# Kernel optimization log

Measured on AMD Instinct MI355X. Metric: run time of the kernel, lower is better.

Reference implementation:

```python
import jax, jax.numpy as jnp
import numpy as np
import math

N_HEADS = 16
D_EMBED = 1024
D_CROSS = 768
FF_DIM = 4096
D_HEAD = D_EMBED // N_HEADS
LN_EPS = 1e-5


def layer_norm(h, g, b):
    mu = jnp.mean(h, axis=-1, keepdims=True)
    var = jnp.var(h, axis=-1, keepdims=True)
    return (h - mu) * jax.lax.rsqrt(var + LN_EPS) * g + b


def mha(q, k, v):
    # q: [B,Sq,D], k/v: [B,Skv,D] -> split heads, attend, merge
    B, Sq, _ = q.shape
    Skv = k.shape[1]
    qh = q.reshape(B, Sq, N_HEADS, D_HEAD).transpose(0, 2, 1, 3)
    kh = k.reshape(B, Skv, N_HEADS, D_HEAD).transpose(0, 2, 1, 3)
    vh = v.reshape(B, Skv, N_HEADS, D_HEAD).transpose(0, 2, 1, 3)
    scores = jnp.einsum('bhqd,bhkd->bhqk', qh, kh) / math.sqrt(D_HEAD)
    attn = jax.nn.softmax(scores, axis=-1)
    out = jnp.einsum('bhqk,bhkd->bhqd', attn, vh)
    return out.transpose(0, 2, 1, 3).reshape(B, Sq, D_EMBED)


def setup_inputs() -> dict:
    key = jax.random.key(0)
    ks = jax.random.split(key, 24)
    s = 0.02
    inp = {
        'x': jax.random.normal(ks[0], (4, 1024, D_EMBED), jnp.float32),
        'y': jax.random.normal(ks[1], (4, 77, D_CROSS), jnp.float32),
        # self-attention in_proj (d_embed -> 3*d_embed) and out_proj
        'w_qkv': jax.random.normal(ks[2], (D_EMBED, 3 * D_EMBED), jnp.float32) * s,
        'b_qkv': jnp.zeros((3 * D_EMBED,), jnp.float32),
        'w_so': jax.random.normal(ks[3], (D_EMBED, D_EMBED), jnp.float32) * s,
        'b_so': jnp.zeros((D_EMBED,), jnp.float32),
        # cross-attention projections
        'w_q': jax.random.normal(ks[4], (D_EMBED, D_EMBED), jnp.float32) * s,
        'b_q': jnp.zeros((D_EMBED,), jnp.float32),
        'w_k': jax.random.normal(ks[5], (D_CROSS, D_EMBED), jnp.float32) * s,
        'b_k': jnp.zeros((D_EMBED,), jnp.float32),
        'w_v': jax.random.normal(ks[6], (D_CROSS, D_EMBED), jnp.float32) * s,
        'b_v': jnp.zeros((D_EMBED,), jnp.float32),
        'w_co': jax.random.normal(ks[7], (D_EMBED, D_EMBED), jnp.float32) * s,
        'b_co': jnp.zeros((D_EMBED,), jnp.float32),
        # 3-layer FFN
        'w1': jax.random.normal(ks[8], (D_EMBED, FF_DIM), jnp.float32) * s,
        'b1': jnp.zeros((FF_DIM,), jnp.float32),
        'w2': jax.random.normal(ks[9], (FF_DIM, FF_DIM), jnp.float32) * s,
        'b2': jnp.zeros((FF_DIM,), jnp.float32),
        'w3': jax.random.normal(ks[10], (FF_DIM, D_EMBED), jnp.float32) * s,
        'b3': jnp.zeros((D_EMBED,), jnp.float32),
        # single shared LayerNorm (used 3 times, as in the torch module)
        'ln_g': jnp.ones((D_EMBED,), jnp.float32),
        'ln_b': jnp.zeros((D_EMBED,), jnp.float32),
    }
    return inp


def reference(x, y, w_qkv, b_qkv, w_so, b_so, w_q, b_q, w_k, b_k, w_v, b_v,
              w_co, b_co, w1, b1, w2, b2, w3, b3, ln_g, ln_b):
    # --- self attention (no causal mask) ---
    qkv = x @ w_qkv + b_qkv
    q, k, v = jnp.split(qkv, 3, axis=-1)
    sa = mha(q, k, v) @ w_so + b_so
    x = layer_norm(x + sa, ln_g, ln_b)
    # --- cross attention ---
    qc = x @ w_q + b_q
    kc = y @ w_k + b_k
    vc = y @ w_v + b_v
    ca = mha(qc, kc, vc) @ w_co + b_co
    x = layer_norm(x + ca, ln_g, ln_b)
    # --- 3-layer FFN with ReLU ---
    h = jax.nn.relu(x @ w1 + b1)
    h = jax.nn.relu(h @ w2 + b2)
    ff = h @ w3 + b3
    x = layer_norm(x + ff, ln_g, ln_b)
    return x
```

## Files before the change

kernel.cpp:

```cpp
#include <hip/hip_runtime.h>
#include <hip/hip_bf16.h>
#include <math.h>

typedef short v8s __attribute__((ext_vector_type(8)));
typedef short v4s __attribute__((ext_vector_type(4)));
typedef float v4f __attribute__((ext_vector_type(4)));

__device__ __forceinline__ unsigned short f2bf(float f) {
  union { float f; unsigned u; } a; a.f = f;
  unsigned u = a.u + 0x7fffu + ((a.u >> 16) & 1u);
  return (unsigned short)(u >> 16);
}

__device__ __forceinline__ void gld_lds16(const unsigned short* g, unsigned short* l) {
  __builtin_amdgcn_global_load_lds(
      (const __attribute__((address_space(1))) void*)g,
      (__attribute__((address_space(3))) void*)l,
      16, 0, 0);
}

__global__ void cvt_f32_bf16(const float* __restrict__ in,
                             unsigned short* __restrict__ out, int n4) {
  int i = blockIdx.x * blockDim.x + threadIdx.x;
  if (i >= n4) return;
  float4 v = reinterpret_cast<const float4*>(in)[i];
  ushort4 o;
  o.x = f2bf(v.x); o.y = f2bf(v.y); o.z = f2bf(v.z); o.w = f2bf(v.w);
  reinterpret_cast<ushort4*>(out)[i] = o;
}

__global__ void cvt_transpose(const float* __restrict__ in,
                              unsigned short* __restrict__ out, int K, int N) {
  __shared__ float t[32][33];
  int bx = blockIdx.x, by = blockIdx.y;
  int tx = threadIdx.x, ty = threadIdx.y;
#pragma unroll
  for (int i = 0; i < 4; i++) {
    int k = by * 32 + ty + i * 8;
    t[ty + i * 8][tx] = in[(size_t)k * N + bx * 32 + tx];
  }
  __syncthreads();
#pragma unroll
  for (int i = 0; i < 4; i++) {
    int n = bx * 32 + ty + i * 8;
    out[(size_t)n * K + by * 32 + tx] = f2bf(t[tx][ty + i * 8]);
  }
}

__global__ __launch_bounds__(256)
void transpose_v(const unsigned short* __restrict__ V,
                 unsigned short* __restrict__ Vt,
                 int rowstride, int batch_rows, int Skv, int kvpad) {
  __shared__ __align__(16) unsigned short t[64][80];
  int ch = blockIdx.x, h = blockIdx.y, b = blockIdx.z;
  int tid = threadIdx.x;
  int sr = tid >> 2, sc = (tid & 3) * 16;
  int gr = ch * 64 + sr;
  v8s v0 = {}, v1 = {};
  if (gr < Skv) {
    const unsigned short* p = V + (size_t)(b * batch_rows + gr) * rowstride + h * 64 + sc;
    v0 = *(const v8s*)p; v1 = *(const v8s*)(p + 8);
  }
  *(v8s*)&t[sr][sc]     = v0;
  *(v8s*)&t[sr][sc + 8] = v1;
  __syncthreads();
  int d  = tid >> 2;
  int k0 = (tid & 3) * 16;
  unsigned short* o = Vt + ((size_t)(b * 16 + h) * 64 + d) * kvpad + ch * 64 + k0;
  v8s o0, o1;
#pragma unroll
  for (int e = 0; e < 8; e++) { o0[e] = t[k0 + e][d]; o1[e] = t[k0 + 8 + e][d]; }
  *(v8s*)o       = o0;
  *(v8s*)(o + 8) = o1;
}

template<bool RELU, bool OUTF, bool OUTB>
__global__ __launch_bounds__(256)
void gemm_bf16(const unsigned short* __restrict__ A,
               const unsigned short* __restrict__ BT,
               const float* __restrict__ bias,
               float* __restrict__ Cf, float* __restrict__ Cf2,
               unsigned short* __restrict__ Cb,
               int M, int N, int Kred, int ld) {
  __shared__ __align__(16) unsigned short lA[128 * 64];
  __shared__ __align__(16) unsigned short lB[128 * 64];
  int tid  = threadIdx.x;
  int lane = tid & 63;
  int wave = tid >> 6;
  int wr = (wave >> 1) * 64;
  int wc = (wave & 1) * 64;
  int quad = lane >> 4;
  int l15  = lane & 15;
  int m0 = blockIdx.y * 128;
  int n0 = blockIdx.x * 128;
  int z  = blockIdx.z;

  const unsigned short* Az = A  + (size_t)z * Kred;
  const unsigned short* Bz = BT + (size_t)z * Kred;
  float* Cfo = z ? Cf2 : Cf;
  const float* biasz = z ? nullptr : bias;

  int srow   = tid >> 3;
  int schunk = (tid & 7) ^ (srow & 7);
  const unsigned short* gA = Az + (size_t)(m0 + srow) * ld + schunk * 8;
  const unsigned short* gB = Bz + (size_t)(n0 + srow) * ld + schunk * 8;
  unsigned short* ldsA = lA + wave * 512;
  unsigned short* ldsB = lB + wave * 512;
  const size_t rowblk = (size_t)32 * ld;

  const v4f vzero = {0.f, 0.f, 0.f, 0.f};
  v4f acc[4][4];
#pragma unroll
  for (int i = 0; i < 4; i++)
#pragma unroll
    for (int j = 0; j < 4; j++) acc[i][j] = vzero;

  for (int k0 = 0; k0 < Kred; k0 += 64) {
#pragma unroll
    for (int i = 0; i < 4; i++) {
      gld_lds16(gA + k0 + i * rowblk, ldsA + i * 2048);
      gld_lds16(gB + k0 + i * rowblk, ldsB + i * 2048);
    }
    __syncthreads();
#pragma unroll
    for (int s = 0; s < 2; s++) {
      v8s aF[4], bF[4];
#pragma unroll
      for (int i = 0; i < 4; i++)
        aF[i] = *(const v8s*)&lA[(wr + i * 16 + l15) * 64 + (((s * 4 + quad) ^ (l15 & 7)) * 8)];
#pragma unroll
      for (int j = 0; j < 4; j++)
        bF[j] = *(const v8s*)&lB[(wc + j * 16 + l15) * 64 + (((s * 4 + quad) ^ (l15 & 7)) * 8)];
#pragma unroll
      for (int i = 0; i < 4; i++)
#pragma unroll
        for (int j = 0; j < 4; j++)
          acc[i][j] = __builtin_amdgcn_mfma_f32_16x16x32_bf16(aF[i], bF[j], acc[i][j], 0, 0, 0);
    }
    __syncthreads();
  }

#pragma unroll
  for (int j = 0; j < 4; j++) {
    int col = n0 + wc + j * 16 + l15;
    float bv = biasz ? biasz[col] : 0.f;
#pragma unroll
    for (int i = 0; i < 4; i++) {
#pragma unroll
      for (int r = 0; r < 4; r++) {
        int row = m0 + wr + i * 16 + quad * 4 + r;
        if (row < M) {
          float v = acc[i][j][r] + bv;
          if (RELU) v = fmaxf(v, 0.f);
          if (OUTF) Cfo[(size_t)row * N + col] = v;
          if (OUTB && !z) Cb[(size_t)row * N + col] = f2bf(v);
        }
      }
    }
  }
}

__global__ __launch_bounds__(256)
void attn_kernel(const unsigned short* __restrict__ Q,
                 const unsigned short* __restrict__ K,
                 const unsigned short* __restrict__ Vt,
                 unsigned short* __restrict__ O,
                 int q_rowstride, int kv_rowstride, int o_rowstride,
                 int q_batch_rows, int kv_batch_rows, int Skv, int kvpad,
                 float scale) {
  __shared__ __align__(16) unsigned short lK[64][72];
  __shared__ __align__(16) unsigned short lV[64][72];
  __shared__ __align__(16) unsigned short lP[4][16][72];
  int tid  = threadIdx.x;
  int lane = tid & 63;
  int wave = tid >> 6;
  int quad = lane >> 4;
  int l15  = lane & 15;
  int qt = blockIdx.x, h = blockIdx.y, b = blockIdx.z;

  const unsigned short* Qb  = Q  + (size_t)b * q_batch_rows * q_rowstride + h * 64;
  const unsigned short* Kb  = K  + (size_t)b * kv_batch_rows * kv_rowstride + h * 64;
  const unsigned short* Vtb = Vt + ((size_t)(b * 16 + h) * 64) * kvpad;

  v8s qf0, qf1;
  {
    const unsigned short* qr = Qb + (size_t)(qt * 64 + wave * 16 + l15) * q_rowstride + quad * 8;
    qf0 = *(const v8s*)(qr);
    qf1 = *(const v8s*)(qr + 32);
  }

  const v4f vzero = {0.f, 0.f, 0.f, 0.f};
  v4f o_acc[4];
#pragma unroll
  for (int t = 0; t < 4; t++) o_acc[t] = vzero;
  float m_r[4], l_r[4];
#pragma unroll
  for (int r = 0; r < 4; r++) { m_r[r] = -1e30f; l_r[r] = 0.f; }

  int sr = tid >> 2;
  int sc = (tid & 3) * 16;

  int nch = (Skv + 63) >> 6;
  for (int ch = 0; ch < nch; ch++) {
    int base = ch * 64;
    int gr = base + sr;
    v8s k0v = {}, k1v = {};
    if (gr < Skv) {
      const unsigned short* kp = Kb + (size_t)gr * kv_rowstride + sc;
      k0v = *(const v8s*)kp;  k1v = *(const v8s*)(kp + 8);
    }
    const unsigned short* vp = Vtb + (size_t)sr * kvpad + base + sc;
    v8s w0 = *(const v8s*)vp;
    v8s w1 = *(const v8s*)(vp + 8);
    __syncthreads();
    *(v8s*)&lK[sr][sc]     = k0v;
    *(v8s*)&lK[sr][sc + 8] = k1v;
    {
      v4s a0 = {w0[0], w0[1], w0[2], w0[3]};
      v4s a1 = {w0[4], w0[5], w0[6], w0[7]};
      v4s a2 = {w1[0], w1[1], w1[2], w1[3]};
      v4s a3 = {w1[4], w1[5], w1[6], w1[7]};
      *(v4s*)&lV[sr][sc]      = a0;
      *(v4s*)&lV[sr][sc + 4]  = a1;
      *(v4s*)&lV[sr][sc + 8]  = a2;
      *(v4s*)&lV[sr][sc + 12] = a3;
    }
    __syncthreads();

    float s[4][4];
#pragma unroll
    for (int t = 0; t < 4; t++) {
      v8s kf0 = *(const v8s*)&lK[t * 16 + l15][quad * 8];
      v8s kf1 = *(const v8s*)&lK[t * 16 + l15][32 + quad * 8];
      v4f sacc = vzero;
      sacc = __builtin_amdgcn_mfma_f32_16x16x32_bf16(qf0, kf0, sacc, 0, 0, 0);
      sacc = __builtin_amdgcn_mfma_f32_16x16x32_bf16(qf1, kf1, sacc, 0, 0, 0);
      int kvpos = base + t * 16 + l15;
      bool ok = kvpos < Skv;
#pragma unroll
      for (int r = 0; r < 4; r++) s[t][r] = ok ? sacc[r] * scale : -1e30f;
    }

#pragma unroll
    for (int r = 0; r < 4; r++) {
      float mx = fmaxf(fmaxf(s[0][r], s[1][r]), fmaxf(s[2][r], s[3][r]));
#pragma unroll
      for (int d = 1; d < 16; d <<= 1) mx = fmaxf(mx, __shfl_xor(mx, d));
      float mnew = fmaxf(m_r[r], mx);
      float alpha = __expf(m_r[r] - mnew);
      float sm = 0.f;
#pragma unroll
      for (int t = 0; t < 4; t++) { s[t][r] = __expf(s[t][r] - mnew); sm += s[t][r]; }
#pragma unroll
      for (int d = 1; d < 16; d <<= 1) sm += __shfl_xor(sm, d);
      l_r[r] = l_r[r] * alpha + sm;
      m_r[r] = mnew;
#pragma unroll
      for (int t = 0; t < 4; t++) o_acc[t][r] *= alpha;
    }

#pragma unroll
    for (int t = 0; t < 4; t++)
#pragma unroll
      for (int r = 0; r < 4; r++)
        lP[wave][quad * 4 + r][t * 16 + l15] = f2bf(s[t][r]);
    v8s pf0 = *(const v8s*)&lP[wave][l15][quad * 8];
    v8s pf1 = *(const v8s*)&lP[wave][l15][32 + quad * 8];
#pragma unroll
    for (int t = 0; t < 4; t++) {
      v8s vf0 = *(const v8s*)&lV[t * 16 + l15][quad * 8];
      v8s vf1 = *(const v8s*)&lV[t * 16 + l15][32 + quad * 8];
      o_acc[t] = __builtin_amdgcn_mfma_f32_16x16x32_bf16(pf0, vf0, o_acc[t], 0, 0, 0);
      o_acc[t] = __builtin_amdgcn_mfma_f32_16x16x32_bf16(pf1, vf1, o_acc[t], 0, 0, 0);
    }
  }

  int orow0 = b * q_batch_rows + qt * 64 + wave * 16;
#pragma unroll
  for (int t = 0; t < 4; t++) {
#pragma unroll
    for (int r = 0; r < 4; r++) {
      float v = o_acc[t][r] / l_r[r];
      O[(size_t)(orow0 + quad * 4 + r) * o_rowstride + h * 64 + t * 16 + l15] = f2bf(v);
    }
  }
}

__global__ __launch_bounds__(256)
void ln_kernel(const float* base, const float* __restrict__ delta,
               const float* __restrict__ delta2,
               const float* __restrict__ g, const float* __restrict__ bb,
               float* outf, unsigned short* __restrict__ outb) {
  __shared__ float red[8];
  int row = blockIdx.x;
  int tid = threadIdx.x;
  float4 vb = ((const float4*)(base  + (size_t)row * 1024))[tid];
  float4 vd = ((const float4*)(delta + (size_t)row * 1024))[tid];
  float v0 = vb.x + vd.x, v1 = vb.y + vd.y, v2 = vb.z + vd.z, v3 = vb.w + vd.w;
  if (delta2) {
    float4 v2d = ((const float4*)(delta2 + (size_t)row * 1024))[tid];
    v0 += v2d.x; v1 += v2d.y; v2 += v2d.z; v3 += v2d.w;
  }
  float s = v0 + v1 + v2 + v3;
  float q = v0 * v0 + v1 * v1 + v2 * v2 + v3 * v3;
#pragma unroll
  for (int d = 1; d < 64; d <<= 1) { s += __shfl_xor(s, d); q += __shfl_xor(q, d); }
  int wave = tid >> 6, lane = tid & 63;
  if (lane == 0) { red[wave] = s; red[4 + wave] = q; }
  __syncthreads();
  s = red[0] + red[1] + red[2] + red[3];
  q = red[4] + red[5] + red[6] + red[7];
  float mean = s * (1.f / 1024.f);
  float var  = q * (1.f / 1024.f) - mean * mean;
  float rstd = rsqrtf(var + 1e-5f);
  float4 gg  = ((const float4*)g)[tid];
  float4 bv  = ((const float4*)bb)[tid];
  float o0 = (v0 - mean) * rstd * gg.x + bv.x;
  float o1 = (v1 - mean) * rstd * gg.y + bv.y;
  float o2 = (v2 - mean) * rstd * gg.z + bv.z;
  float o3 = (v3 - mean) * rstd * gg.w + bv.w;
  if (outf) {
    float4 o; o.x = o0; o.y = o1; o.z = o2; o.w = o3;
    ((float4*)(outf + (size_t)row * 1024))[tid] = o;
  }
  if (outb) {
    ushort4 u; u.x = f2bf(o0); u.y = f2bf(o1); u.z = f2bf(o2); u.w = f2bf(o3);
    ((ushort4*)(outb + (size_t)row * 1024))[tid] = u;
  }
}

extern "C" void kernel_launch(void* const* d_in, const int* in_sizes, int n_in,
                              void* d_out, int out_size, void* d_ws, size_t ws_size,
                              hipStream_t stream) {
  const float* x     = (const float*)d_in[0];
  const float* y     = (const float*)d_in[1];
  const float* w_qkv = (const float*)d_in[2];
  const float* b_qkv = (const float*)d_in[3];
  const float* w_so  = (const float*)d_in[4];
  const float* b_so  = (const float*)d_in[5];
  const float* w_q   = (const float*)d_in[6];
  const float* b_q   = (const float*)d_in[7];
  const float* w_k   = (const float*)d_in[8];
  const float* b_k   = (const float*)d_in[9];
  const float* w_v   = (const float*)d_in[10];
  const float* b_v   = (const float*)d_in[11];
  const float* w_co  = (const float*)d_in[12];
  const float* b_co  = (const float*)d_in[13];
  const float* w1    = (const float*)d_in[14];
  const float* b1    = (const float*)d_in[15];
  const float* w2    = (const float*)d_in[16];
  const float* b2    = (const float*)d_in[17];
  const float* w3    = (const float*)d_in[18];
  const float* b3    = (const float*)d_in[19];
  const float* ln_g  = (const float*)d_in[20];
  const float* ln_b  = (const float*)d_in[21];

  char* ws = (char*)d_ws;
  auto US = [&](size_t off) { return (unsigned short*)(ws + off); };
  auto FP = [&](size_t off) { return (float*)(ws + off); };

  constexpr size_t o_wqkv = 0;
  constexpr size_t o_wso  = o_wqkv + 3072ull * 1024 * 2;
  constexpr size_t o_wq   = o_wso  + 1024ull * 1024 * 2;
  constexpr size_t o_wk   = o_wq   + 1024ull * 1024 * 2;
  constexpr size_t o_wv   = o_wk   + 1024ull * 768 * 2;
  constexpr size_t o_wco  = o_wv   + 1024ull * 768 * 2;
  constexpr size_t o_w1   = o_wco  + 1024ull * 1024 * 2;
  constexpr size_t o_w2   = o_w1   + 4096ull * 1024 * 2;
  constexpr size_t o_w3   = o_w2   + 4096ull * 4096 * 2;
  constexpr size_t o_xf   = o_w3   + 1024ull * 4096 * 2;
  constexpr size_t o_xbf  = o_xf   + 4096ull * 1024 * 4;
  constexpr size_t o_ybf  = o_xbf  + 4096ull * 1024 * 2;
  constexpr size_t o_dlt  = o_ybf  + 308ull * 768 * 2;
  constexpr size_t o_R1   = o_dlt  + 4096ull * 1024 * 4;
  constexpr size_t o_attn = o_R1   + 4096ull * 3072 * 2;
  constexpr size_t o_R2   = o_attn + 4096ull * 1024 * 2;
  constexpr size_t o_qc  = o_R1;
  constexpr size_t o_kc  = o_R1 + 4096ull * 1024 * 2;
  constexpr size_t o_vc  = o_kc + 308ull * 1024 * 2;
  constexpr size_t o_h1  = o_R1;
  constexpr size_t o_h2  = o_R2;
  constexpr size_t o_dlt2 = o_R1;
  constexpr size_t o_vtS = o_R2;
  constexpr size_t o_vtC = o_R2 + 4ull * 16 * 64 * 1024 * 2;

  dim3 tb(32, 8);
  cvt_transpose<<<dim3(96, 32),  tb, 0, stream>>>(w_qkv, US(o_wqkv), 1024, 3072);
  cvt_transpose<<<dim3(32, 32),  tb, 0, stream>>>(w_so,  US(o_wso),  1024, 1024);
  cvt_transpose<<<dim3(32, 32),  tb, 0, stream>>>(w_q,   US(o_wq),   1024, 1024);
  cvt_transpose<<<dim3(32, 24),  tb, 0, stream>>>(w_k,   US(o_wk),   768,  1024);
  cvt_transpose<<<dim3(32, 24),  tb, 0, stream>>>(w_v,   US(o_wv),   768,  1024);
  cvt_transpose<<<dim3(32, 32),  tb, 0, stream>>>(w_co,  US(o_wco),  1024, 1024);
  cvt_transpose<<<dim3(128, 32), tb, 0, stream>>>(w1,    US(o_w1),   1024, 4096);
  cvt_transpose<<<dim3(128, 128),tb, 0, stream>>>(w2,    US(o_w2),   4096, 4096);
  cvt_transpose<<<dim3(32, 128), tb, 0, stream>>>(w3,    US(o_w3),   4096, 1024);

  cvt_f32_bf16<<<4096, 256, 0, stream>>>(x, US(o_xbf), 4096 * 1024 / 4);
  cvt_f32_bf16<<<231, 256, 0, stream>>>(y, US(o_ybf), 4 * 77 * 768 / 4);

  gemm_bf16<false, false, true><<<dim3(24, 32, 1), 256, 0, stream>>>(
      US(o_xbf), US(o_wqkv), b_qkv, nullptr, nullptr, US(o_R1), 4096, 3072, 1024, 1024);
  transpose_v<<<dim3(16, 16, 4), 256, 0, stream>>>(
      US(o_R1) + 2048, US(o_vtS), 3072, 1024, 1024, 1024);
  attn_kernel<<<dim3(16, 16, 4), 256, 0, stream>>>(
      US(o_R1), US(o_R1) + 1024, US(o_vtS), US(o_attn),
      3072, 3072, 1024, 1024, 1024, 1024, 1024, 0.125f);
  gemm_bf16<false, true, false><<<dim3(8, 32, 2), 256, 0, stream>>>(
      US(o_attn), US(o_wso), b_so, FP(o_dlt), FP(o_dlt2), nullptr, 4096, 1024, 512, 1024);
  ln_kernel<<<4096, 256, 0, stream>>>(x, FP(o_dlt), FP(o_dlt2), ln_g, ln_b,
                                      FP(o_xf), US(o_xbf));

  gemm_bf16<false, false, true><<<dim3(8, 32, 1), 256, 0, stream>>>(
      US(o_xbf), US(o_wq), b_q, nullptr, nullptr, US(o_qc), 4096, 1024, 1024, 1024);
  gemm_bf16<false, false, true><<<dim3(8, 3, 1), 256, 0, stream>>>(
      US(o_ybf), US(o_wk), b_k, nullptr, nullptr, US(o_kc), 308, 1024, 768, 768);
  gemm_bf16<false, false, true><<<dim3(8, 3, 1), 256, 0, stream>>>(
      US(o_ybf), US(o_wv), b_v, nullptr, nullptr, US(o_vc), 308, 1024, 768, 768);
  transpose_v<<<dim3(2, 16, 4), 256, 0, stream>>>(
      US(o_vc), US(o_vtC), 1024, 77, 77, 128);
  attn_kernel<<<dim3(16, 16, 4), 256, 0, stream>>>(
      US(o_qc), US(o_kc), US(o_vtC), US(o_attn),
      1024, 1024, 1024, 1024, 77, 77, 128, 0.125f);
  gemm_bf16<false, true, false><<<dim3(8, 32, 2), 256, 0, stream>>>(
      US(o_attn), US(o_wco), b_co, FP(o_dlt), FP(o_dlt2), nullptr, 4096, 1024, 512, 1024);
  ln_kernel<<<4096, 256, 0, stream>>>(FP(o_xf), FP(o_dlt), FP(o_dlt2), ln_g, ln_b,
                                      FP(o_xf), US(o_xbf));

  gemm_bf16<true, false, true><<<dim3(32, 32, 1), 256, 0, stream>>>(
      US(o_xbf), US(o_w1), b1, nullptr, nullptr, US(o_h1), 4096, 4096, 1024, 1024);
  gemm_bf16<true, false, true><<<dim3(32, 32, 1), 256, 0, stream>>>(
      US(o_h1), US(o_w2), b2, nullptr, nullptr, US(o_h2), 4096, 4096, 4096, 4096);
  gemm_bf16<false, true, false><<<dim3(8, 32, 2), 256, 0, stream>>>(
      US(o_h2), US(o_w3), b3, FP(o_dlt), FP(o_dlt2), nullptr, 4096, 1024, 2048, 4096);
  ln_kernel<<<4096, 256, 0, stream>>>(FP(o_xf), FP(o_dlt), FP(o_dlt2), ln_g, ln_b,
                                      (float*)d_out, nullptr);
}
```

Before: 804.6 us.

## Add 256x256-tile double-buffered bf16 GEMM for QKV and FFN1/FFN2

Adds a new 512-thread GEMM kernel with 256x256 output tiles, double-buffered LDS filled by direct global-to-LDS loads, XOR-swizzled LDS layout, and interleaved MFMA phases with priority boosting and explicit barriers. It replaces the 128x128 kernel for the QKV projection and the first two FFN layers, aiming for more data reuse per tile and overlap of loads with MFMA work. The larger tile gives fewer blocks (192 or 256) over the GPU's CUs, so occupancy and tail effects may limit the benefit, and the vmcnt and barrier choreography is fragile.

```diff
diff --git a/kernel.cpp b/kernel.cpp
--- a/kernel.cpp
+++ b/kernel.cpp
@@ -72,6 +72,152 @@
   for (int e = 0; e < 8; e++) { o0[e] = t[k0 + e][d]; o1[e] = t[k0 + 8 + e][d]; }
   *(v8s*)o       = o0;
   *(v8s*)(o + 8) = o1;
+}
+
+template<bool RELU>
+__global__ __launch_bounds__(512, 2)
+void gemm256(const unsigned short* __restrict__ A,
+             const unsigned short* __restrict__ BT,
+             const float* __restrict__ bias,
+             unsigned short* __restrict__ Cb,
+             int M, int N, int K, int lda, int ldb) {
+  __shared__ __align__(16) unsigned short lA[2][2][8192];
+  __shared__ __align__(16) unsigned short lB[2][2][8192];
+  int tid  = threadIdx.x;
+  int lane = tid & 63;
+  int wave = tid >> 6;
+  int wrow = wave >> 2;
+  int wcol = wave & 3;
+  int quad = lane >> 4;
+  int l15  = lane & 15;
+  int m0 = blockIdx.y * 256;
+  int n0 = blockIdx.x * 256;
+  int NT = K >> 6;
+
+  int srow  = wave * 16 + (lane >> 2);
+  int scol8 = ((lane & 3) ^ quad) << 3;
+  const unsigned short* gA = A  + (size_t)(m0 + srow) * lda + scol8;
+  const unsigned short* gB = BT + (size_t)(n0 + srow) * ldb + scol8;
+  const size_t rowblkA = (size_t)128 * lda;
+  const size_t rowblkB = (size_t)128 * ldb;
+
+  auto stageA = [&](int U, int kh) {
+    unsigned short* d = &lA[U & 1][kh][wave * 512];
+    const unsigned short* s = gA + (size_t)U * 64 + kh * 32;
+    gld_lds16(s, d);
+    gld_lds16(s + rowblkA, d + 4096);
+  };
+  auto stageB = [&](int U, int kh) {
+    unsigned short* d = &lB[U & 1][kh][wave * 512];
+    const unsigned short* s = gB + (size_t)U * 64 + kh * 32;
+    gld_lds16(s, d);
+    gld_lds16(s + rowblkB, d + 4096);
+  };
+
+  int rsw   = (l15 >> 2) & 3;
+  int chOff = ((quad ^ rsw) << 3);
+  int aBase = (wrow * 128 + l15) * 32 + chOff;
+  int bBase = (wcol * 64  + l15) * 32 + chOff;
+
+  const v4f vzero = {0.f, 0.f, 0.f, 0.f};
+  v4f acc[8][4];
+#pragma unroll
+  for (int i = 0; i < 8; i++)
+#pragma unroll
+    for (int j = 0; j < 4; j++) acc[i][j] = vzero;
+
+  stageB(0, 0); stageA(0, 0); stageA(0, 1); stageB(0, 1);
+  if (NT > 1) {
+    stageB(1, 0); stageA(1, 0);
+    asm volatile("s_waitcnt vmcnt(4)" ::: "memory");
+  } else {
+    asm volatile("s_waitcnt vmcnt(0)" ::: "memory");
+  }
+  __builtin_amdgcn_s_barrier();
+  __builtin_amdgcn_sched_barrier(0);
+
+  for (int U = 0; U < NT; ++U) {
+    int c = U & 1;
+    v8s aF[4], bF[4];
+
+#pragma unroll
+    for (int n = 0; n < 4; n++) bF[n] = *(const v8s*)&lB[c][0][bBase + n * 512];
+#pragma unroll
+    for (int m = 0; m < 4; m++) aF[m] = *(const v8s*)&lA[c][0][aBase + m * 512];
+    if (U + 1 < NT) stageA(U + 1, 1);
+    __builtin_amdgcn_s_barrier();
+    __builtin_amdgcn_s_setprio(1);
+#pragma unroll
+    for (int m = 0; m < 4; m++)
+#pragma unroll
+      for (int n = 0; n < 4; n++)
+        acc[m][n] = __builtin_amdgcn_mfma_f32_16x16x32_bf16(aF[m], bF[n], acc[m][n], 0, 0, 0);
+    __builtin_amdgcn_s_setprio(0);
+    __builtin_amdgcn_s_barrier();
+
+#pragma unroll
+    for (int m = 0; m < 4; m++) aF[m] = *(const v8s*)&lA[c][0][aBase + (4 + m) * 512];
+    if (U + 1 < NT) stageB(U + 1, 1);
+    __builtin_amdgcn_s_barrier();
+    __builtin_amdgcn_s_setprio(1);
+#pragma unroll
+    for (int m = 0; m < 4; m++)
+#pragma unroll
+      for (int n = 0; n < 4; n++)
+        acc[4 + m][n] = __builtin_amdgcn_mfma_f32_16x16x32_bf16(aF[m], bF[n], acc[4 + m][n], 0, 0, 0);
+    __builtin_amdgcn_s_setprio(0);
+    __builtin_amdgcn_s_barrier();
+
+#pragma unroll
+    for (int n = 0; n < 4; n++) bF[n] = *(const v8s*)&lB[c][1][bBase + n * 512];
+#pragma unroll
+    for (int m = 0; m < 4; m++) aF[m] = *(const v8s*)&lA[c][1][aBase + m * 512];
+    if (U + 2 < NT) stageB(U + 2, 0);
+    __builtin_amdgcn_s_barrier();
+    __builtin_amdgcn_s_setprio(1);
+#pragma unroll
+    for (int m = 0; m < 4; m++)
+#pragma unroll
+      for (int n = 0; n < 4; n++)
+        acc[m][n] = __builtin_amdgcn_mfma_f32_16x16x32_bf16(aF[m], bF[n], acc[m][n], 0, 0, 0);
+    __builtin_amdgcn_s_setprio(0);
+    __builtin_amdgcn_s_barrier();
+
+#pragma unroll
+    for (int m = 0; m < 4; m++) aF[m] = *(const v8s*)&lA[c][1][aBase + (4 + m) * 512];
+    if (U + 2 < NT) stageA(U + 2, 0);
+    __builtin_amdgcn_s_barrier();
+    __builtin_amdgcn_s_setprio(1);
+#pragma unroll
+    for (int m = 0; m < 4; m++)
+#pragma unroll
+      for (int n = 0; n < 4; n++)
+        acc[4 + m][n] = __builtin_amdgcn_mfma_f32_16x16x32_bf16(aF[m], bF[n], acc[4 + m][n], 0, 0, 0);
+    __builtin_amdgcn_s_setprio(0);
+    if (U + 2 < NT) asm volatile("s_waitcnt vmcnt(4)" ::: "memory");
+    else            asm volatile("s_waitcnt vmcnt(0)" ::: "memory");
+    __builtin_amdgcn_s_barrier();
+    __builtin_amdgcn_sched_barrier(0);
+  }
+
+#pragma unroll
+  for (int j = 0; j < 4; j++) {
+    int col = n0 + wcol * 64 + j * 16 + l15;
+    float bv = bias[col];
+#pragma unroll
+    for (int i = 0; i < 8; i++) {
+      int rb = m0 + wrow * 128 + (i >> 2) * 64 + (i & 3) * 16 + quad * 4;
+#pragma unroll
+      for (int r = 0; r < 4; r++) {
+        int row = rb + r;
+        if (row < M) {
+          float v = acc[i][j][r] + bv;
+          if (RELU) v = fmaxf(v, 0.f);
+          Cb[(size_t)row * N + col] = f2bf(v);
+        }
+      }
+    }
+  }
 }
 
 template<bool RELU, bool OUTF, bool OUTB>
@@ -398,8 +544,8 @@
   cvt_f32_bf16<<<4096, 256, 0, stream>>>(x, US(o_xbf), 4096 * 1024 / 4);
   cvt_f32_bf16<<<231, 256, 0, stream>>>(y, US(o_ybf), 4 * 77 * 768 / 4);
 
-  gemm_bf16<false, false, true><<<dim3(24, 32, 1), 256, 0, stream>>>(
-      US(o_xbf), US(o_wqkv), b_qkv, nullptr, nullptr, US(o_R1), 4096, 3072, 1024, 1024);
+  gemm256<false><<<dim3(12, 16), 512, 0, stream>>>(
+      US(o_xbf), US(o_wqkv), b_qkv, US(o_R1), 4096, 3072, 1024, 1024, 1024);
   transpose_v<<<dim3(16, 16, 4), 256, 0, stream>>>(
       US(o_R1) + 2048, US(o_vtS), 3072, 1024, 1024, 1024);
   attn_kernel<<<dim3(16, 16, 4), 256, 0, stream>>>(
@@ -426,10 +572,10 @@
   ln_kernel<<<4096, 256, 0, stream>>>(FP(o_xf), FP(o_dlt), FP(o_dlt2), ln_g, ln_b,
                                       FP(o_xf), US(o_xbf));
 
-  gemm_bf16<true, false, true><<<dim3(32, 32, 1), 256, 0, stream>>>(
-      US(o_xbf), US(o_w1), b1, nullptr, nullptr, US(o_h1), 4096, 4096, 1024, 1024);
-  gemm_bf16<true, false, true><<<dim3(32, 32, 1), 256, 0, stream>>>(
-      US(o_h1), US(o_w2), b2, nullptr, nullptr, US(o_h2), 4096, 4096, 4096, 4096);
+  gemm256<true><<<dim3(16, 16), 512, 0, stream>>>(
+      US(o_xbf), US(o_w1), b1, US(o_h1), 4096, 4096, 1024, 1024, 1024);
+  gemm256<true><<<dim3(16, 16), 512, 0, stream>>>(
+      US(o_h1), US(o_w2), b2, US(o_h2), 4096, 4096, 4096, 4096, 4096);
   gemm_bf16<false, true, false><<<dim3(8, 32, 2), 256, 0, stream>>>(
       US(o_h2), US(o_w3), b3, FP(o_dlt), FP(o_dlt2), nullptr, 4096, 1024, 2048, 4096);
   ln_kernel<<<4096, 256, 0, stream>>>(FP(o_xf), FP(o_dlt), FP(o_dlt2), ln_g, ln_b,
```

Result: faster. 774.9 us (-3.7%).
